# Kernel tuning notes

Measured on AMD Instinct MI355X. Metric: run time of the kernel, lower is better.

## Reference

```python
import math
import jax, jax.numpy as jnp
import numpy as np

NUM_FRAMES = 512
NUM_ANIMALS = 4
N_HEAD = 8
N_EMBD = 512
B = 2
T = NUM_FRAMES * NUM_ANIMALS  # 2048


def _block_causal_mask():
    # tril over frames, full attention within each frame across animals
    tril = jnp.tril(jnp.ones((NUM_FRAMES, NUM_FRAMES), dtype=jnp.float32))
    return jnp.kron(tril, jnp.ones((NUM_ANIMALS, NUM_ANIMALS), dtype=jnp.float32))  # [T, T]


def setup_inputs() -> dict:
    key = jax.random.key(0)
    ks = jax.random.split(key, 6)
    s = 1.0 / math.sqrt(N_EMBD)
    return {
        "x": jax.random.normal(ks[0], (B, T, N_EMBD), dtype=jnp.float32),
        "mask": jnp.ones((B, T), dtype=jnp.int32),
        "Wq": jax.random.normal(ks[1], (N_EMBD, N_EMBD), dtype=jnp.float32) * s,
        "bq": jnp.zeros((N_EMBD,), dtype=jnp.float32),
        "Wk": jax.random.normal(ks[2], (N_EMBD, N_EMBD), dtype=jnp.float32) * s,
        "bk": jnp.zeros((N_EMBD,), dtype=jnp.float32),
        "Wv": jax.random.normal(ks[3], (N_EMBD, N_EMBD), dtype=jnp.float32) * s,
        "bv": jnp.zeros((N_EMBD,), dtype=jnp.float32),
        "Wp": jax.random.normal(ks[4], (N_EMBD, N_EMBD), dtype=jnp.float32) * s,
        "bp": jnp.zeros((N_EMBD,), dtype=jnp.float32),
    }


def reference(x, mask, Wq, bq, Wk, bk, Wv, bv, Wp, bp):
    b, t, c = x.shape
    h, d = N_HEAD, c // N_HEAD
    scale = 1.0 / math.sqrt(d)

    def heads(w, bias):
        return (x @ w + bias).reshape(b, t, h, d).transpose(0, 2, 1, 3)  # [B,H,T,D]

    q = heads(Wq, bq)
    k = heads(Wk, bk)
    v = heads(Wv, bv)

    att = jnp.einsum("bhqd,bhkd->bhqk", q, k) * scale  # [B,H,T,T]
    block = _block_causal_mask()  # [T,T]
    allowed = block[None, None, :, :] * mask[:, None, None, :].astype(jnp.float32)
    att = jnp.where(allowed == 0, -jnp.inf, att)
    att = jax.nn.softmax(att, axis=-1)
    # attn_pdrop = resid_pdrop = 0.0 -> dropout is identity
    y = jnp.einsum("bhqk,bhkd->bhqd", att, v)  # [B,H,T,D]
    y = y.transpose(0, 2, 1, 3).reshape(b, t, c)
    return y @ Wp + bp
```

## Files before the change

kernel.cpp:

```cpp
#include <hip/hip_runtime.h>


typedef unsigned short u16;
typedef unsigned int   u32;
typedef __bf16 bf16x8 __attribute__((ext_vector_type(8)));
typedef float  f32x4  __attribute__((ext_vector_type(4)));
typedef short  s16x4  __attribute__((ext_vector_type(4)));

static __device__ __forceinline__ u16 f2b(float f) {
  __bf16 h = (__bf16)f;
  return __builtin_bit_cast(u16, h);
}
static __device__ __forceinline__ u32 pack2(float a, float b) {
  return (u32)f2b(a) | ((u32)f2b(b) << 16);
}
static __device__ __forceinline__ bf16x8 ld_bf16x8(const u16* p) {
  uint4 u = *(const uint4*)p;
  return __builtin_bit_cast(bf16x8, u);
}
static __device__ __forceinline__ f32x4 mfma32(bf16x8 a, bf16x8 b, f32x4 c) {
  return __builtin_amdgcn_mfma_f32_16x16x32_bf16(a, b, c, 0, 0, 0);
}
static __device__ __forceinline__ f32x4 mfma16(s16x4 a, s16x4 b, f32x4 c) {
  return __builtin_amdgcn_mfma_f32_16x16x16bf16_1k(a, b, c, 0, 0, 0);
}
static __device__ __forceinline__ void gload16(const u16* g, u16* l) {
  __builtin_amdgcn_global_load_lds(
      (const __attribute__((address_space(1))) void*)g,
      (__attribute__((address_space(3))) void*)l, 16, 0, 0);
}

__global__ __launch_bounds__(256) void k_cvt_x(const float* __restrict__ x,
                                               u16* __restrict__ xb) {
  int i = blockIdx.x * 256 + threadIdx.x;
  const float4* s = (const float4*)x;
  float4 a = s[2 * i], b = s[2 * i + 1];
  uint4 o;
  o.x = pack2(a.x, a.y);
  o.y = pack2(a.z, a.w);
  o.z = pack2(b.x, b.y);
  o.w = pack2(b.z, b.w);
  ((uint4*)xb)[i] = o;
}

__global__ __launch_bounds__(256) void k_cvt_w(
    const float* __restrict__ Wq, const float* __restrict__ Wk,
    const float* __restrict__ Wv, const float* __restrict__ Wp,
    u16* __restrict__ oq, u16* __restrict__ ok,
    u16* __restrict__ ov, u16* __restrict__ op) {
  const int z = blockIdx.z;
  const float* src = (z == 0) ? Wq : (z == 1) ? Wk : (z == 2) ? Wv : Wp;
  u16* dst = (z == 0) ? oq : (z == 1) ? ok : (z == 2) ? ov : op;
  __shared__ float t[32][33];
  const int tx = threadIdx.x, ty = threadIdx.y;
  const int n0 = blockIdx.x * 32, k0 = blockIdx.y * 32;
#pragma unroll
  for (int i = 0; i < 4; ++i)
    t[ty + i * 8][tx] = src[(size_t)(k0 + ty + i * 8) * 512 + n0 + tx];
  __syncthreads();
#pragma unroll
  for (int i = 0; i < 4; ++i)
    dst[(size_t)(n0 + ty + i * 8) * 512 + k0 + tx] = f2b(t[tx][ty + i * 8]);
}

template <int BM>
__global__ __launch_bounds__(512) void k_gemm(
    const u16* __restrict__ A,
    const u16* __restrict__ Bt_0, const u16* __restrict__ Bt_1,
    const u16* __restrict__ Bt_2,
    const float* __restrict__ bias_0, const float* __restrict__ bias_1,
    const float* __restrict__ bias_2,
    void* out_0, void* out_1, void* out_2,
    int mode_0, int mode_1, int mode_2) {
  const int z = blockIdx.z;
  const u16* Bt = (z == 0) ? Bt_0 : (z == 1) ? Bt_1 : Bt_2;
  const float* bias = (z == 0) ? bias_0 : (z == 1) ? bias_1 : bias_2;
  void* outp = (z == 0) ? out_0 : (z == 1) ? out_1 : out_2;
  const int mode = (z == 0) ? mode_0 : (z == 1) ? mode_1 : mode_2;

  constexpr int MI = BM / 32;
  const int tid = threadIdx.x, lane = tid & 63, w = tid >> 6;
  const int wm = w >> 2, wn = w & 3;
  const int lr = lane & 15, lg = lane >> 4;
  const int m0 = blockIdx.y * BM, n0 = blockIdx.x * 128;

  __shared__ __align__(16) u16 As[2][BM * 64];
  __shared__ __align__(16) u16 Bs[2][128 * 64];

  f32x4 acc[MI][2];
  const f32x4 fz = {0.f, 0.f, 0.f, 0.f};
#pragma unroll
  for (int mi = 0; mi < MI; ++mi)
#pragma unroll
    for (int ni = 0; ni < 2; ++ni) acc[mi][ni] = fz;

  const int lro = lane >> 3;
  const int lch = (lane & 7) ^ (lro & 7);

  auto stage = [&](int kk, int buf) {
#pragma unroll
    for (int j = 0; j < BM / 64; ++j) {
      const int r0 = w * (BM / 8) + j * 8;
      gload16(A + (size_t)(m0 + r0 + lro) * 512 + kk + lch * 8,
              &As[buf][r0 * 64]);
    }
#pragma unroll
    for (int j = 0; j < 2; ++j) {
      const int r0 = w * 16 + j * 8;
      gload16(Bt + (size_t)(n0 + r0 + lro) * 512 + kk + lch * 8,
              &Bs[buf][r0 * 64]);
    }
  };

  stage(0, 0);
  __syncthreads();
  for (int kt = 0; kt < 8; ++kt) {
    if (kt + 1 < 8) stage((kt + 1) * 64, (kt + 1) & 1);
    const int buf = kt & 1;
#pragma unroll
    for (int kc = 0; kc < 2; ++kc) {
      bf16x8 af[MI], bfv[2];
#pragma unroll
      for (int mi = 0; mi < MI; ++mi) {
        const int r = wm * (BM / 2) + mi * 16 + lr;
        af[mi] = ld_bf16x8(&As[buf][r * 64 + (((kc * 4 + lg) ^ (r & 7)) << 3)]);
      }
#pragma unroll
      for (int ni = 0; ni < 2; ++ni) {
        const int r = wn * 32 + ni * 16 + lr;
        bfv[ni] = ld_bf16x8(&Bs[buf][r * 64 + (((kc * 4 + lg) ^ (r & 7)) << 3)]);
      }
#pragma unroll
      for (int mi = 0; mi < MI; ++mi)
#pragma unroll
        for (int ni = 0; ni < 2; ++ni)
          acc[mi][ni] = mfma32(af[mi], bfv[ni], acc[mi][ni]);
    }
    __syncthreads();
  }

#pragma unroll
  for (int mi = 0; mi < MI; ++mi) {
#pragma unroll
    for (int ni = 0; ni < 2; ++ni) {
      const int mbase = m0 + wm * (BM / 2) + mi * 16 + lg * 4;
      const int n = n0 + wn * 32 + ni * 16 + lr;
      const float bsv = bias[n];
      if (mode == 0) {
        u16* o = (u16*)outp;
#pragma unroll
        for (int i = 0; i < 4; ++i)
          o[(size_t)(mbase + i) * 512 + n] = f2b(acc[mi][ni][i] + bsv);
      } else if (mode == 1) {
        u16* o = (u16*)outp;
        const int bb = mbase >> 11, t = mbase & 2047;
        const size_t rowb = ((size_t)(bb * 8 + (n >> 6)) * 64 + (n & 63)) * 2048;
        *(u32*)(o + rowb + t)     = pack2(acc[mi][ni][0] + bsv, acc[mi][ni][1] + bsv);
        *(u32*)(o + rowb + t + 2) = pack2(acc[mi][ni][2] + bsv, acc[mi][ni][3] + bsv);
      } else {
        float* o = (float*)outp;
#pragma unroll
        for (int i = 0; i < 4; ++i)
          o[(size_t)(mbase + i) * 512 + n] = acc[mi][ni][i] + bsv;
      }
    }
  }
}

__global__ __launch_bounds__(256) void k_attn(
    const u16* __restrict__ Q, const u16* __restrict__ K,
    const u16* __restrict__ Vt, const int* __restrict__ mask,
    u16* __restrict__ y) {
  const int b = blockIdx.z, h = blockIdx.y;
  const int qt = 31 - blockIdx.x;
  const int tid = threadIdx.x, lane = tid & 63, w = tid >> 6;
  const int lr = lane & 15, lg = lane >> 4;
  const int q0 = qt * 64 + w * 16;
  const int fq = (q0 + lr) >> 2;

  __shared__ __align__(16) u16 Ks[2][64 * 64];
  __shared__ __align__(16) u16 Vs[2][64 * 64];

  const size_t brow = (size_t)b * 2048;
  const u16* qp = Q + (brow + q0 + lr) * 512 + h * 64 + lg * 8;
  const bf16x8 qf0 = ld_bf16x8(qp);
  const bf16x8 qf1 = ld_bf16x8(qp + 32);
  const int* maskp = mask + b * 2048;

  const f32x4 fz = {0.f, 0.f, 0.f, 0.f};
  f32x4 yacc[4];
#pragma unroll
  for (int dt = 0; dt < 4; ++dt) yacc[dt] = fz;
  float mrun = -__builtin_inff(), lrun = 0.f;

  const int lro = lane >> 3;
  const int lch = (lane & 7) ^ (lro & 7);
  const u16* kgbase = K + brow * 512 + h * 64 + lch * 8;
  const u16* vgbase = Vt + ((size_t)(b * 8 + h) * 64) * 2048 + lch * 8;

  auto stage = [&](int c, int buf) {
    const int c0 = c << 6;
#pragma unroll
    for (int j = 0; j < 2; ++j) {
      const int r0 = w * 16 + j * 8;
      gload16(kgbase + (size_t)(c0 + r0 + lro) * 512, &Ks[buf][r0 * 64]);
    }
#pragma unroll
    for (int j = 0; j < 2; ++j) {
      const int r0 = w * 16 + j * 8;
      gload16(vgbase + (size_t)(r0 + lro) * 2048 + c0, &Vs[buf][r0 * 64]);
    }
  };

  auto compute = [&](int c, int buf) {
    const int c0 = c << 6;
    f32x4 s[4];
#pragma unroll
    for (int kt = 0; kt < 4; ++kt) {
      const int r = kt * 16 + lr;
      s[kt] = mfma32(ld_bf16x8(&Ks[buf][r * 64 + ((lg ^ (r & 7)) << 3)]), qf0, fz);
    }
#pragma unroll
    for (int kt = 0; kt < 4; ++kt) {
      const int r = kt * 16 + lr;
      s[kt] = mfma32(ld_bf16x8(&Ks[buf][r * 64 + (((lg + 4) ^ (r & 7)) << 3)]),
                     qf1, s[kt]);
    }

    float sv[4][4];
    float tm = -__builtin_inff();
#pragma unroll
    for (int kt = 0; kt < 4; ++kt) {
      const int k0 = c0 + kt * 16;
      const bool kill = ((k0 >> 2) + lg) > fq;
      const int4 mv = *(const int4*)&maskp[k0 + lg * 4];
#pragma unroll
      for (int i = 0; i < 4; ++i) {
        const int mvi = (i == 0) ? mv.x : (i == 1) ? mv.y : (i == 2) ? mv.z : mv.w;
        float v = s[kt][i] * 0.125f;
        if (kill || mvi == 0) v = -__builtin_inff();
        sv[kt][i] = v;
        tm = fmaxf(tm, v);
      }
    }
    tm = fmaxf(tm, __shfl_xor(tm, 16));
    tm = fmaxf(tm, __shfl_xor(tm, 32));

    const float mnew = fmaxf(mrun, tm);
    const float msafe = (mnew == -__builtin_inff()) ? 0.f : mnew;
    const float alpha =
        (mrun == -__builtin_inff()) ? 0.f : __expf(mrun - msafe);

    float psum = 0.f;
    s16x4 pf[4];
#pragma unroll
    for (int kt = 0; kt < 4; ++kt) {
#pragma unroll
      for (int i = 0; i < 4; ++i) {
        const float pv = __expf(sv[kt][i] - msafe);
        psum += pv;
        pf[kt][i] = (short)f2b(pv);
      }
    }
    psum += __shfl_xor(psum, 16);
    psum += __shfl_xor(psum, 32);
    lrun = lrun * alpha + psum;
    mrun = mnew;

#pragma unroll
    for (int dt = 0; dt < 4; ++dt) {
#pragma unroll
      for (int i = 0; i < 4; ++i) yacc[dt][i] *= alpha;
#pragma unroll
      for (int kt = 0; kt < 4; ++kt) {
        const int r = dt * 16 + lr;
        const int ch = kt * 2 + (lg >> 1);
        const uint2 vv = *(const uint2*)&Vs[buf][r * 64 +
                                                 ((ch ^ (r & 7)) << 3) +
                                                 ((lg & 1) << 2)];
        yacc[dt] = mfma16(__builtin_bit_cast(s16x4, vv), pf[kt], yacc[dt]);
      }
    }
  };

  const int nchunk = qt + 1;
  stage(0, 0);
  __syncthreads();
  for (int c = 0; c < nchunk; ++c) {
    if (c + 1 < nchunk) stage(c + 1, (c + 1) & 1);
    compute(c, c & 1);
    __syncthreads();
  }

  const float inv = 1.f / lrun;
#pragma unroll
  for (int dt = 0; dt < 4; ++dt) {
    u32* p2 = (u32*)(y + (brow + q0 + lr) * 512 + h * 64 + dt * 16 + lg * 4);
    p2[0] = pack2(yacc[dt][0] * inv, yacc[dt][1] * inv);
    p2[1] = pack2(yacc[dt][2] * inv, yacc[dt][3] * inv);
  }
}

extern "C" void kernel_launch(void* const* d_in, const int* in_sizes, int n_in,
                              void* d_out, int out_size, void* d_ws,
                              size_t ws_size, hipStream_t stream) {
  const float* x  = (const float*)d_in[0];
  const int* mask = (const int*)d_in[1];
  const float* Wq = (const float*)d_in[2];
  const float* bq = (const float*)d_in[3];
  const float* Wk = (const float*)d_in[4];
  const float* bk = (const float*)d_in[5];
  const float* Wv = (const float*)d_in[6];
  const float* bv = (const float*)d_in[7];
  const float* Wp = (const float*)d_in[8];
  const float* bp = (const float*)d_in[9];

  char* ws = (char*)d_ws;
  u16* xb  = (u16*)(ws);
  u16* wqt = (u16*)(ws + (4u << 20));
  u16* wkt = (u16*)(ws + (4u << 20) + 524288u);
  u16* wvt = (u16*)(ws + (5u << 20));
  u16* wpt = (u16*)(ws + (5u << 20) + 524288u);
  u16* Qb  = (u16*)(ws + (6u << 20));
  u16* Kb  = (u16*)(ws + (10u << 20));
  u16* Vtb = (u16*)(ws + (14u << 20));
  u16* yb  = (u16*)(ws + (18u << 20));

  k_cvt_x<<<dim3(1024), dim3(256), 0, stream>>>(x, xb);
  k_cvt_w<<<dim3(16, 16, 4), dim3(32, 8), 0, stream>>>(Wq, Wk, Wv, Wp, wqt, wkt,
                                                       wvt, wpt);
  k_gemm<128><<<dim3(4, 32, 3), dim3(512), 0, stream>>>(
      xb, wqt, wkt, wvt, bq, bk, bv, (void*)Qb, (void*)Kb, (void*)Vtb, 0, 0, 1);
  k_attn<<<dim3(32, 8, 2), dim3(256), 0, stream>>>(Qb, Kb, Vtb, mask, yb);
  k_gemm<64><<<dim3(4, 64, 1), dim3(512), 0, stream>>>(
      yb, wpt, wpt, wpt, bp, bp, bp, d_out, d_out, d_out, 2, 2, 2);
}
```

Measured before the change: 158.7 us.

## Triple-buffer GEMM and attention loads, fold softmax scale into Q, lazy rescale

Both the GEMM and attention kernels move from double to triple buffering, using explicit vmcnt waits and a single barrier per iteration so that loads run two stages ahead. The GEMM N tile is halved to 64 to launch more blocks, and occupancy hints are added. The 1/sqrt(d)*log2(e) factor is folded into the Q projection so attention can use exp2 without a per-score multiply. The online-softmax rescale is skipped unless the max grows by more than 8, which cuts multiplies but lets the exponentials grow up to 2^8 before renormalisation, with some precision risk. Mask loads are also hoisted ahead of the QK MFMAs.

```diff
diff --git a/kernel.cpp b/kernel.cpp
--- a/kernel.cpp
+++ b/kernel.cpp
@@ -6,6 +6,9 @@
 typedef __bf16 bf16x8 __attribute__((ext_vector_type(8)));
 typedef float  f32x4  __attribute__((ext_vector_type(4)));
 typedef short  s16x4  __attribute__((ext_vector_type(4)));
+
+#define WAITV(n) asm volatile("s_waitcnt vmcnt(" #n ")" ::: "memory")
+#define BARRIER() asm volatile("s_barrier" ::: "memory")
 
 static __device__ __forceinline__ u16 f2b(float f) {
   __bf16 h = (__bf16)f;
@@ -63,36 +66,38 @@
     dst[(size_t)(n0 + ty + i * 8) * 512 + k0 + tx] = f2b(t[tx][ty + i * 8]);
 }
 
-template <int BM>
-__global__ __launch_bounds__(512) void k_gemm(
+template <int BM, int BN>
+__global__ __launch_bounds__(512, 4) void k_gemm(
     const u16* __restrict__ A,
     const u16* __restrict__ Bt_0, const u16* __restrict__ Bt_1,
     const u16* __restrict__ Bt_2,
     const float* __restrict__ bias_0, const float* __restrict__ bias_1,
     const float* __restrict__ bias_2,
+    float scl_0, float scl_1, float scl_2,
     void* out_0, void* out_1, void* out_2,
     int mode_0, int mode_1, int mode_2) {
   const int z = blockIdx.z;
   const u16* Bt = (z == 0) ? Bt_0 : (z == 1) ? Bt_1 : Bt_2;
   const float* bias = (z == 0) ? bias_0 : (z == 1) ? bias_1 : bias_2;
+  const float scl = (z == 0) ? scl_0 : (z == 1) ? scl_1 : scl_2;
   void* outp = (z == 0) ? out_0 : (z == 1) ? out_1 : out_2;
   const int mode = (z == 0) ? mode_0 : (z == 1) ? mode_1 : mode_2;
 
-  constexpr int MI = BM / 32;
+  constexpr int MI = BM / 32, NI = BN / 64;
   const int tid = threadIdx.x, lane = tid & 63, w = tid >> 6;
   const int wm = w >> 2, wn = w & 3;
   const int lr = lane & 15, lg = lane >> 4;
-  const int m0 = blockIdx.y * BM, n0 = blockIdx.x * 128;
-
-  __shared__ __align__(16) u16 As[2][BM * 64];
-  __shared__ __align__(16) u16 Bs[2][128 * 64];
-
-  f32x4 acc[MI][2];
+  const int m0 = blockIdx.y * BM, n0 = blockIdx.x * BN;
+
+  __shared__ __align__(16) u16 As[3][BM * 64];
+  __shared__ __align__(16) u16 Bs[3][BN * 64];
+
+  f32x4 acc[MI][NI];
   const f32x4 fz = {0.f, 0.f, 0.f, 0.f};
 #pragma unroll
   for (int mi = 0; mi < MI; ++mi)
 #pragma unroll
-    for (int ni = 0; ni < 2; ++ni) acc[mi][ni] = fz;
+    for (int ni = 0; ni < NI; ++ni) acc[mi][ni] = fz;
 
   const int lro = lane >> 3;
   const int lch = (lane & 7) ^ (lro & 7);
@@ -105,52 +110,60 @@
               &As[buf][r0 * 64]);
     }
 #pragma unroll
-    for (int j = 0; j < 2; ++j) {
-      const int r0 = w * 16 + j * 8;
+    for (int j = 0; j < BN / 64; ++j) {
+      const int r0 = w * (BN / 8) + j * 8;
       gload16(Bt + (size_t)(n0 + r0 + lro) * 512 + kk + lch * 8,
               &Bs[buf][r0 * 64]);
     }
   };
 
   stage(0, 0);
-  __syncthreads();
+  stage(64, 1);
+  int cur = 0, nx2 = 2;
   for (int kt = 0; kt < 8; ++kt) {
-    if (kt + 1 < 8) stage((kt + 1) * 64, (kt + 1) & 1);
-    const int buf = kt & 1;
+    if (kt < 7) {
+      if constexpr (BM / 64 + BN / 64 == 3) WAITV(3); else WAITV(2);
+    } else {
+      WAITV(0);
+    }
+    BARRIER();
+    if (kt + 2 < 8) stage((kt + 2) * 64, nx2);
+
 #pragma unroll
     for (int kc = 0; kc < 2; ++kc) {
-      bf16x8 af[MI], bfv[2];
+      bf16x8 af[MI], bfv[NI];
 #pragma unroll
       for (int mi = 0; mi < MI; ++mi) {
         const int r = wm * (BM / 2) + mi * 16 + lr;
-        af[mi] = ld_bf16x8(&As[buf][r * 64 + (((kc * 4 + lg) ^ (r & 7)) << 3)]);
-      }
-#pragma unroll
-      for (int ni = 0; ni < 2; ++ni) {
-        const int r = wn * 32 + ni * 16 + lr;
-        bfv[ni] = ld_bf16x8(&Bs[buf][r * 64 + (((kc * 4 + lg) ^ (r & 7)) << 3)]);
+        af[mi] = ld_bf16x8(&As[cur][r * 64 + (((kc * 4 + lg) ^ (r & 7)) << 3)]);
+      }
+#pragma unroll
+      for (int ni = 0; ni < NI; ++ni) {
+        const int r = (wn * NI + ni) * 16 + lr;
+        bfv[ni] = ld_bf16x8(&Bs[cur][r * 64 + (((kc * 4 + lg) ^ (r & 7)) << 3)]);
       }
 #pragma unroll
       for (int mi = 0; mi < MI; ++mi)
 #pragma unroll
-        for (int ni = 0; ni < 2; ++ni)
+        for (int ni = 0; ni < NI; ++ni)
           acc[mi][ni] = mfma32(af[mi], bfv[ni], acc[mi][ni]);
     }
-    __syncthreads();
+    cur = (cur == 2) ? 0 : cur + 1;
+    nx2 = (nx2 == 2) ? 0 : nx2 + 1;
   }
 
 #pragma unroll
   for (int mi = 0; mi < MI; ++mi) {
 #pragma unroll
-    for (int ni = 0; ni < 2; ++ni) {
+    for (int ni = 0; ni < NI; ++ni) {
       const int mbase = m0 + wm * (BM / 2) + mi * 16 + lg * 4;
-      const int n = n0 + wn * 32 + ni * 16 + lr;
+      const int n = n0 + (wn * NI + ni) * 16 + lr;
       const float bsv = bias[n];
       if (mode == 0) {
         u16* o = (u16*)outp;
 #pragma unroll
         for (int i = 0; i < 4; ++i)
-          o[(size_t)(mbase + i) * 512 + n] = f2b(acc[mi][ni][i] + bsv);
+          o[(size_t)(mbase + i) * 512 + n] = f2b((acc[mi][ni][i] + bsv) * scl);
       } else if (mode == 1) {
         u16* o = (u16*)outp;
         const int bb = mbase >> 11, t = mbase & 2047;
@@ -167,7 +180,7 @@
   }
 }
 
-__global__ __launch_bounds__(256) void k_attn(
+__global__ __launch_bounds__(256, 3) void k_attn(
     const u16* __restrict__ Q, const u16* __restrict__ K,
     const u16* __restrict__ Vt, const int* __restrict__ mask,
     u16* __restrict__ y) {
@@ -177,9 +190,10 @@
   const int lr = lane & 15, lg = lane >> 4;
   const int q0 = qt * 64 + w * 16;
   const int fq = (q0 + lr) >> 2;
-
-  __shared__ __align__(16) u16 Ks[2][64 * 64];
-  __shared__ __align__(16) u16 Vs[2][64 * 64];
+  const float NINF = -__builtin_inff();
+
+  __shared__ __align__(16) u16 Ks[3][64 * 64];
+  __shared__ __align__(16) u16 Vs[3][64 * 64];
 
   const size_t brow = (size_t)b * 2048;
   const u16* qp = Q + (brow + q0 + lr) * 512 + h * 64 + lg * 8;
@@ -191,7 +205,7 @@
   f32x4 yacc[4];
 #pragma unroll
   for (int dt = 0; dt < 4; ++dt) yacc[dt] = fz;
-  float mrun = -__builtin_inff(), lrun = 0.f;
+  float mrun = NINF, lrun = 0.f;
 
   const int lro = lane >> 3;
   const int lch = (lane & 7) ^ (lro & 7);
@@ -214,6 +228,11 @@
 
   auto compute = [&](int c, int buf) {
     const int c0 = c << 6;
+    int4 mv4[4];
+#pragma unroll
+    for (int kt = 0; kt < 4; ++kt)
+      mv4[kt] = *(const int4*)&maskp[c0 + kt * 16 + lg * 4];
+
     f32x4 s[4];
 #pragma unroll
     for (int kt = 0; kt < 4; ++kt) {
@@ -228,17 +247,17 @@
     }
 
     float sv[4][4];
-    float tm = -__builtin_inff();
+    float tm = NINF;
 #pragma unroll
     for (int kt = 0; kt < 4; ++kt) {
       const int k0 = c0 + kt * 16;
       const bool kill = ((k0 >> 2) + lg) > fq;
-      const int4 mv = *(const int4*)&maskp[k0 + lg * 4];
+      const int4 mv = mv4[kt];
 #pragma unroll
       for (int i = 0; i < 4; ++i) {
         const int mvi = (i == 0) ? mv.x : (i == 1) ? mv.y : (i == 2) ? mv.z : mv.w;
-        float v = s[kt][i] * 0.125f;
-        if (kill || mvi == 0) v = -__builtin_inff();
+        float v = s[kt][i];
+        if (kill || mvi == 0) v = NINF;
         sv[kt][i] = v;
         tm = fmaxf(tm, v);
       }
@@ -246,10 +265,17 @@
     tm = fmaxf(tm, __shfl_xor(tm, 16));
     tm = fmaxf(tm, __shfl_xor(tm, 32));
 
-    const float mnew = fmaxf(mrun, tm);
-    const float msafe = (mnew == -__builtin_inff()) ? 0.f : mnew;
-    const float alpha =
-        (mrun == -__builtin_inff()) ? 0.f : __expf(mrun - msafe);
+    if (__any(tm > mrun + 8.f)) {
+      const float mnew = fmaxf(mrun, tm);
+      const float alpha = (mrun == NINF) ? 0.f : exp2f(mrun - mnew);
+      lrun *= alpha;
+#pragma unroll
+      for (int dt = 0; dt < 4; ++dt)
+#pragma unroll
+        for (int i = 0; i < 4; ++i) yacc[dt][i] *= alpha;
+      mrun = mnew;
+    }
+    const float msafe = (mrun == NINF) ? 0.f : mrun;
 
     float psum = 0.f;
     s16x4 pf[4];
@@ -257,20 +283,17 @@
     for (int kt = 0; kt < 4; ++kt) {
 #pragma unroll
       for (int i = 0; i < 4; ++i) {
-        const float pv = __expf(sv[kt][i] - msafe);
+        const float pv = exp2f(sv[kt][i] - msafe);
         psum += pv;
         pf[kt][i] = (short)f2b(pv);
       }
     }
     psum += __shfl_xor(psum, 16);
     psum += __shfl_xor(psum, 32);
-    lrun = lrun * alpha + psum;
-    mrun = mnew;
+    lrun += psum;
 
 #pragma unroll
     for (int dt = 0; dt < 4; ++dt) {
-#pragma unroll
-      for (int i = 0; i < 4; ++i) yacc[dt][i] *= alpha;
 #pragma unroll
       for (int kt = 0; kt < 4; ++kt) {
         const int r = dt * 16 + lr;
@@ -285,11 +308,15 @@
 
   const int nchunk = qt + 1;
   stage(0, 0);
-  __syncthreads();
+  if (nchunk > 1) stage(1, 1);
+  int cur = 0, nx2 = 2;
   for (int c = 0; c < nchunk; ++c) {
-    if (c + 1 < nchunk) stage(c + 1, (c + 1) & 1);
-    compute(c, c & 1);
-    __syncthreads();
+    if (c + 1 < nchunk) WAITV(4); else WAITV(0);
+    BARRIER();
+    if (c + 2 < nchunk) stage(c + 2, nx2);
+    compute(c, cur);
+    cur = (cur == 2) ? 0 : cur + 1;
+    nx2 = (nx2 == 2) ? 0 : nx2 + 1;
   }
 
   const float inv = 1.f / lrun;
@@ -326,12 +353,16 @@
   u16* Vtb = (u16*)(ws + (14u << 20));
   u16* yb  = (u16*)(ws + (18u << 20));
 
+  const float SCLQ = 0.125f * 1.4426950408889634f;
+
   k_cvt_x<<<dim3(1024), dim3(256), 0, stream>>>(x, xb);
   k_cvt_w<<<dim3(16, 16, 4), dim3(32, 8), 0, stream>>>(Wq, Wk, Wv, Wp, wqt, wkt,
                                                        wvt, wpt);
-  k_gemm<128><<<dim3(4, 32, 3), dim3(512), 0, stream>>>(
-      xb, wqt, wkt, wvt, bq, bk, bv, (void*)Qb, (void*)Kb, (void*)Vtb, 0, 0, 1);
+  k_gemm<128, 64><<<dim3(8, 32, 3), dim3(512), 0, stream>>>(
+      xb, wqt, wkt, wvt, bq, bk, bv, SCLQ, 1.f, 1.f,
+      (void*)Qb, (void*)Kb, (void*)Vtb, 0, 0, 1);
   k_attn<<<dim3(32, 8, 2), dim3(256), 0, stream>>>(Qb, Kb, Vtb, mask, yb);
-  k_gemm<64><<<dim3(4, 64, 1), dim3(512), 0, stream>>>(
-      yb, wpt, wpt, wpt, bp, bp, bp, d_out, d_out, d_out, 2, 2, 2);
-}
+  k_gemm<64, 64><<<dim3(8, 64, 1), dim3(512), 0, stream>>>(
+      yb, wpt, wpt, wpt, bp, bp, bp, 1.f, 1.f, 1.f,
+      d_out, d_out, d_out, 2, 2, 2);
+}
```

After: 164.4 us. 1.04x slower.
